# Optimization experiments

Hardware: AMD Instinct MI355X
Metric: run time of the kernel (lower is better)

The kernel has to match this reference:

```python
import jax, jax.numpy as jnp
import numpy as np

TOPK = 5
MAX_CANDIDATES = 32
MAX_LAG_CAP = 168
LN_EPS = 1e-5


def setup_inputs() -> dict:
    key = jax.random.key(0)
    ks = jax.random.split(key, 8)
    B, L, D = 32, 2048, 512
    x = jax.random.normal(ks[0], (B, L, D), dtype=jnp.float32)
    conv_w0 = jax.random.normal(ks[1], (D, 1, 3), dtype=jnp.float32) * 0.1
    conv_w1 = jax.random.normal(ks[2], (D, 1, 5), dtype=jnp.float32) * 0.1
    conv_w2 = jax.random.normal(ks[3], (D, 1, 7), dtype=jnp.float32) * 0.1
    proj_w = jax.random.normal(ks[4], (D, 2 * D), dtype=jnp.float32) * (1.0 / np.sqrt(2 * D))
    proj_b = jnp.zeros((D,), dtype=jnp.float32)
    ln_g = jnp.ones((D,), dtype=jnp.float32)
    ln_b = jnp.zeros((D,), dtype=jnp.float32)
    return {"x": x, "conv_w0": conv_w0, "conv_w1": conv_w1, "conv_w2": conv_w2,
            "proj_w": proj_w, "proj_b": proj_b, "ln_g": ln_g, "ln_b": ln_b}


def _depthwise_conv(x_ncl, w, dilation):
    # x_ncl: [B, D, L], w: [D, 1, k] (torch depthwise layout == OIH with groups=D)
    k = w.shape[-1]
    pad = (k // 2) * dilation
    return jax.lax.conv_general_dilated(
        x_ncl, w, window_strides=(1,), padding=[(pad, pad)],
        rhs_dilation=(dilation,), dimension_numbers=("NCH", "OIH", "NCH"),
        feature_group_count=x_ncl.shape[1])


def _autocorr(x):
    # x: [B, L, D] -> weighted sum of circular shifts at top-k lags
    B, L, D = x.shape
    xm = x.mean(axis=-1)  # [B, L]
    max_lag = min(L - 1, MAX_LAG_CAP)
    num = min(max_lag, MAX_CANDIDATES)
    lags = np.linspace(1, max_lag, num).astype(np.int64)  # static candidate lags
    # score per lag: mean_t xm[:, t] * xm[:, t+lag]
    scores = jnp.stack(
        [(xm[:, : L - int(l)] * xm[:, int(l):]).mean(axis=1) for l in lags], axis=1)  # [B, num]
    k = min(TOPK, num)
    vals, idx = jax.lax.top_k(scores, k)  # [B, k]
    denom = vals.sum(axis=1, keepdims=True) + 1e-6
    # scatter normalized top-k weights onto candidate-lag axis
    w = jnp.zeros((B, num), x.dtype).at[jnp.arange(B)[:, None], idx].add(vals / denom)  # [B, num]
    out = jnp.zeros_like(x)
    for li, lag in enumerate(lags):
        out = out + w[:, li, None, None] * jnp.roll(x, int(lag), axis=1)
    return out


def reference(x, conv_w0, conv_w1, conv_w2, proj_w, proj_b, ln_g, ln_b):
    # depthwise multi-dilation conv branch
    x_T = jnp.transpose(x, (0, 2, 1))  # [B, D, L]
    y_conv = (_depthwise_conv(x_T, conv_w0, 1)
              + _depthwise_conv(x_T, conv_w1, 2)
              + _depthwise_conv(x_T, conv_w2, 4))
    y_conv = jnp.transpose(y_conv, (0, 2, 1))  # [B, L, D]
    # autocorrelation branch
    y_auto = _autocorr(x)
    # project (dropout is identity in eval) + residual + layernorm
    y = jnp.concatenate([y_conv, y_auto], axis=-1)  # [B, L, 2D]
    y = jnp.einsum("bld,od->blo", y, proj_w) + proj_b
    h = x + y
    mu = h.mean(axis=-1, keepdims=True)
    var = h.var(axis=-1, keepdims=True)
    return (h - mu) * jax.lax.rsqrt(var + LN_EPS) * ln_g + ln_b
```

## Files before the change

### kernel.cpp

```cpp
#include <hip/hip_runtime.h>

#define DEVI __device__ __forceinline__

typedef __attribute__((ext_vector_type(8))) short s16x8;
typedef __attribute__((ext_vector_type(4))) float f32x4;

__device__ __constant__ int LAGS_C[32] = {
    1,6,11,17,22,27,33,38,44,49,54,60,65,71,76,81,
    87,92,97,103,108,114,119,124,130,135,141,146,151,157,162,168};

DEVI unsigned short f2bf(float f) {
  unsigned u = __float_as_uint(f);
  return (unsigned short)((u + 0x7FFFu + ((u >> 16) & 1u)) >> 16);
}
DEVI unsigned pk2(float a, float b) {
  return (unsigned)f2bf(a) | ((unsigned)f2bf(b) << 16);
}

DEVI f32x4 mfma16(s16x8 a, s16x8 b, f32x4 c) {
  asm("v_mfma_f32_16x16x32_bf16 %0, %1, %2, %0" : "+v"(c) : "v"(a), "v"(b));
  return c;
}

DEVI void gl_lds16(const void* g, void* l) {
  __builtin_amdgcn_global_load_lds(
      (const __attribute__((address_space(1))) unsigned int*)g,
      (__attribute__((address_space(3))) unsigned int*)l, 16, 0, 0);
}

__global__ __launch_bounds__(256) void k_mean(const float* __restrict__ x,
                                              float* __restrict__ xm) {
  int row = blockIdx.x * 4 + (threadIdx.x >> 6);
  int lane = threadIdx.x & 63;
  const float4* p = (const float4*)(x + (size_t)row * 512 + lane * 8);
  float4 a = p[0], bq = p[1];
  float s = a.x + a.y + a.z + a.w + bq.x + bq.y + bq.z + bq.w;
#pragma unroll
  for (int off = 32; off; off >>= 1) s += __shfl_xor(s, off, 64);
  if (lane == 0) xm[row] = s * (1.0f / 512.0f);
}

__global__ __launch_bounds__(256) void k_cvt(const float* __restrict__ pw,
                                             unsigned short* __restrict__ pwb) {
  int i = (blockIdx.x * 256 + threadIdx.x) * 4;
  float4 v = *(const float4*)(pw + i);
  ushort4 o;
  o.x = f2bf(v.x); o.y = f2bf(v.y); o.z = f2bf(v.z); o.w = f2bf(v.w);
  *(ushort4*)(pwb + i) = o;
}

__global__ __launch_bounds__(256) void k_scores(const float* __restrict__ xm,
                                                float* __restrict__ scores) {
  __shared__ float xs[2048];
  int b = blockIdx.x, tid = threadIdx.x;
  const float4* src = (const float4*)(xm + b * 2048);
  float4* dst = (float4*)xs;
  for (int i = tid; i < 512; i += 256) dst[i] = src[i];
  __syncthreads();
  int wid = tid >> 6, lane = tid & 63;
  for (int j = 0; j < 8; ++j) {
    int li = wid * 8 + j;
    int lag = LAGS_C[li];
    int n = 2048 - lag;
    float p = 0.f;
    for (int t = lane; t < n; t += 64) p += xs[t] * xs[t + lag];
#pragma unroll
    for (int off = 32; off; off >>= 1) p += __shfl_xor(p, off, 64);
    if (lane == 0) scores[b * 32 + li] = p / (float)n;
  }
}

__global__ __launch_bounds__(64) void k_topk(const float* __restrict__ scores,
                                             int* __restrict__ lsel,
                                             float* __restrict__ wsel) {
  int b = threadIdx.x;
  if (b >= 32) return;
  unsigned used = 0;
  int idxs[5];
  float vals[5];
  for (int j = 0; j < 5; ++j) {
    float best = -3.402823466e38f;
    int bi = 0;
    for (int i = 0; i < 32; ++i) {
      float v = scores[b * 32 + i];
      if (!((used >> i) & 1u) && v > best) { best = v; bi = i; }
    }
    used |= 1u << bi;
    idxs[j] = bi;
    vals[j] = best;
  }
  float denom = vals[0] + vals[1] + vals[2] + vals[3] + vals[4] + 1e-6f;
  for (int j = 0; j < 5; ++j) {
    lsel[b * 5 + j] = LAGS_C[idxs[j]];
    wsel[b * 5 + j] = vals[j] / denom;
  }
}

__global__ __launch_bounds__(256) void k_prep(
    const float* __restrict__ x, const float* __restrict__ cw0,
    const float* __restrict__ cw1, const float* __restrict__ cw2,
    const int* __restrict__ lsel, const float* __restrict__ wsel,
    unsigned short* __restrict__ Ab, int b0) {
  __shared__ float xs[88][128];
  __shared__ float cws[15][128];
  const int tid = threadIdx.x;
  const int brel = blockIdx.x >> 7;
  const int t = blockIdx.x & 127;
  const int rt = t >> 2, chg = t & 3;
  const int b = b0 + brel;
  const int l0 = rt << 6;
  const int d0 = chg << 7;
  const float* xb = x + (size_t)b * (2048 * 512);

  for (int idx = tid; idx < 88 * 32; idx += 256) {
    int row = idx >> 5, c4 = idx & 31;
    int l = l0 - 12 + row;
    float4 v = make_float4(0.f, 0.f, 0.f, 0.f);
    if (l >= 0 && l < 2048) v = *(const float4*)(xb + (size_t)l * 512 + d0 + c4 * 4);
    *(float4*)(&xs[row][c4 * 4]) = v;
  }
  for (int idx = tid; idx < 15 * 128; idx += 256) {
    int tap = idx >> 7, ch = idx & 127;
    int d = d0 + ch;
    float v;
    if (tap < 3) v = cw0[d * 3 + tap];
    else if (tap < 8) v = cw1[d * 5 + (tap - 3)];
    else v = cw2[d * 7 + (tap - 8)];
    cws[tap][ch] = v;
  }
  int lag[5];
  float wv[5];
#pragma unroll
  for (int j = 0; j < 5; ++j) {
    lag[j] = lsel[b * 5 + j];
    wv[j] = wsel[b * 5 + j];
  }
  __syncthreads();

  const int ch4 = tid & 31, rbase = tid >> 5;
  constexpr int COFF[15] = {-1, 0, 1, -4, -2, 0, 2, 4, -12, -8, -4, 0, 4, 8, 12};
#pragma unroll 1
  for (int p = 0; p < 8; ++p) {
    int r = p * 8 + rbase;
    float a0 = 0, a1 = 0, a2 = 0, a3 = 0;
#pragma unroll
    for (int tap = 0; tap < 15; ++tap) {
      float4 xv = *(const float4*)(&xs[r + 12 + COFF[tap]][ch4 * 4]);
      float4 wv4 = *(const float4*)(&cws[tap][ch4 * 4]);
      a0 = fmaf(wv4.x, xv.x, a0);
      a1 = fmaf(wv4.y, xv.y, a1);
      a2 = fmaf(wv4.z, xv.z, a2);
      a3 = fmaf(wv4.w, xv.w, a3);
    }
    unsigned short* Arow = Ab + (size_t)(brel * 2048 + l0 + r) * 1024;
    uint2 oc;
    oc.x = pk2(a0, a1);
    oc.y = pk2(a2, a3);
    *(uint2*)(Arow + d0 + ch4 * 4) = oc;
    float s0 = 0, s1 = 0, s2 = 0, s3 = 0;
    int l = l0 + r;
#pragma unroll
    for (int j = 0; j < 5; ++j) {
      int sl = (l - lag[j]) & 2047;
      float4 v = *(const float4*)(xb + (size_t)sl * 512 + d0 + ch4 * 4);
      float w = wv[j];
      s0 = fmaf(w, v.x, s0);
      s1 = fmaf(w, v.y, s1);
      s2 = fmaf(w, v.z, s2);
      s3 = fmaf(w, v.w, s3);
    }
    uint2 oa;
    oa.x = pk2(s0, s1);
    oa.y = pk2(s2, s3);
    *(uint2*)(Arow + 512 + d0 + ch4 * 4) = oa;
  }
}

__global__ __launch_bounds__(512, 1) void k_gemm(
    const unsigned short* __restrict__ Ab, const unsigned short* __restrict__ pwb,
    const float* __restrict__ x, const float* __restrict__ pb,
    const float* __restrict__ lng, const float* __restrict__ lnb,
    float* __restrict__ out, size_t mbase) {
  __shared__ __align__(16) char smem[81920];
  char* Asm = smem;
  char* Bsm = smem + 16384;
  float2* red = (float2*)smem;
  float2* rstat = (float2*)(smem + 4096);

  const int tid = threadIdx.x;
  const int lane = tid & 63;
  const int wid = tid >> 6;
  const int wr = wid >> 2, wc = wid & 3;
  const int lr = lane & 15, g4 = lane >> 4;
  const int m0 = blockIdx.x << 7;

  const int sr = tid >> 2;
  const int ssl = (tid & 3) ^ ((sr >> 1) & 3);
  const unsigned short* aSrc = Ab + (size_t)(m0 + sr) * 1024 + ssl * 8;
  const unsigned short* bSrc0 = pwb + (size_t)sr * 1024 + ssl * 8;

  f32x4 acc[4][8];
#pragma unroll
  for (int m = 0; m < 4; ++m)
#pragma unroll
    for (int n = 0; n < 8; ++n) acc[m][n] = f32x4{0.f, 0.f, 0.f, 0.f};

  const int swsl = (g4 ^ ((lr >> 1) & 3)) << 4;
  const int aoff = (wr * 64 + lr) * 64 + swsl;
  const int boff = (wc * 128 + lr) * 64 + swsl;

#define STAGE(bufi, kt)                                                   \
  do {                                                                    \
    gl_lds16(aSrc + (kt) * 32, Asm + (bufi) * 8192 + wid * 1024);         \
    _Pragma("unroll") for (int i = 0; i < 4; ++i)                         \
        gl_lds16(bSrc0 + (size_t)i * 131072 + (kt) * 32,                  \
                 Bsm + (bufi) * 32768 + i * 8192 + wid * 1024);           \
  } while (0)

  STAGE(0, 0);
  __syncthreads();
#pragma unroll 1
  for (int kt = 0; kt < 32; ++kt) {
    const int cur = kt & 1;
    if (kt + 1 < 32) STAGE(cur ^ 1, kt + 1);
    const char* ab = Asm + cur * 8192;
    const char* bb = Bsm + cur * 32768;
    s16x8 af[4];
#pragma unroll
    for (int m = 0; m < 4; ++m) af[m] = *(const s16x8*)(ab + aoff + m * 1024);
#pragma unroll
    for (int n = 0; n < 8; ++n) {
      s16x8 bf = *(const s16x8*)(bb + boff + n * 1024);
#pragma unroll
      for (int m = 0; m < 4; ++m) acc[m][n] = mfma16(af[m], bf, acc[m][n]);
    }
    __syncthreads();
  }
#undef STAGE

  float pbv[8], gv[8], bv[8];
#pragma unroll
  for (int n = 0; n < 8; ++n) {
    int c = wc * 128 + n * 16 + lr;
    pbv[n] = pb[c];
    gv[n] = lng[c];
    bv[n] = lnb[c];
  }
#pragma unroll
  for (int m = 0; m < 4; ++m) {
#pragma unroll
    for (int reg = 0; reg < 4; ++reg) {
      int row = wr * 64 + m * 16 + g4 * 4 + reg;
      const float* xp = x + (mbase + m0 + row) * 512 + wc * 128 + lr;
      float s1 = 0.f, s2 = 0.f;
#pragma unroll
      for (int n = 0; n < 8; ++n) {
        float h = acc[m][n][reg] + pbv[n] + xp[n * 16];
        acc[m][n][reg] = h;
        s1 += h;
        s2 += h * h;
      }
#pragma unroll
      for (int off = 1; off < 16; off <<= 1) {
        s1 += __shfl_xor(s1, off, 64);
        s2 += __shfl_xor(s2, off, 64);
      }
      if (lr == 0) red[row * 4 + wc] = make_float2(s1, s2);
    }
  }
  __syncthreads();
  if (tid < 128) {
    float s1 = 0.f, s2 = 0.f;
#pragma unroll
    for (int w4 = 0; w4 < 4; ++w4) {
      float2 p = red[tid * 4 + w4];
      s1 += p.x;
      s2 += p.y;
    }
    float mu = s1 * (1.f / 512.f);
    float var = s2 * (1.f / 512.f) - mu * mu;
    rstat[tid] = make_float2(mu, rsqrtf(var + 1e-5f));
  }
  __syncthreads();
#pragma unroll
  for (int m = 0; m < 4; ++m) {
#pragma unroll
    for (int reg = 0; reg < 4; ++reg) {
      int row = wr * 64 + m * 16 + g4 * 4 + reg;
      float2 st = rstat[row];
      float* op = out + (mbase + m0 + row) * 512 + wc * 128 + lr;
#pragma unroll
      for (int n = 0; n < 8; ++n)
        op[n * 16] = (acc[m][n][reg] - st.x) * st.y * gv[n] + bv[n];
    }
  }
}

extern "C" void kernel_launch(void* const* d_in, const int* in_sizes, int n_in,
                              void* d_out, int out_size, void* d_ws, size_t ws_size,
                              hipStream_t stream) {
  const float* x = (const float*)d_in[0];
  const float* cw0 = (const float*)d_in[1];
  const float* cw1 = (const float*)d_in[2];
  const float* cw2 = (const float*)d_in[3];
  const float* pw = (const float*)d_in[4];
  const float* pb = (const float*)d_in[5];
  const float* lng = (const float*)d_in[6];
  const float* lnb = (const float*)d_in[7];
  float* out = (float*)d_out;

  char* ws = (char*)d_ws;
  float* xm = (float*)ws;
  float* scores = (float*)(ws + 262144);
  int* lsel = (int*)(ws + 266240);
  float* wsel = (float*)(ws + 266880);
  unsigned short* pwb = (unsigned short*)(ws + 267520);
  unsigned short* Ab = (unsigned short*)(ws + 1316096);

  size_t avail = ws_size > 1316096 ? ws_size - 1316096 : 0;
  int nch = 1;
  while (nch < 32 && ((size_t)134217728 / nch) > avail) nch <<= 1;
  int bs = 32 / nch;

  k_mean<<<16384, 256, 0, stream>>>(x, xm);
  k_cvt<<<512, 256, 0, stream>>>(pw, pwb);
  k_scores<<<32, 256, 0, stream>>>(xm, scores);
  k_topk<<<1, 64, 0, stream>>>(scores, lsel, wsel);
  for (int c = 0; c < nch; ++c) {
    int b0 = c * bs;
    k_prep<<<bs * 128, 256, 0, stream>>>(x, cw0, cw1, cw2, lsel, wsel, Ab, b0);
    k_gemm<<<bs * 16, 512, 0, stream>>>(Ab, pwb, x, pb, lng, lnb, out,
                                        (size_t)b0 * 2048);
  }
}
```

Measured before the change: 472.9 us.

## Split prep into conv/autocorr kernels, drop batch chunking, retile GEMM to 32 rows

Replaces the combined prep kernel with a separate depthwise-conv kernel that also writes a bf16 copy of x, plus an autocorrelation kernel that gathers the lagged rows from that bf16 copy. The GEMM changes from 128-row tiles with LDS-staged B to 32-row tiles with 256 threads, where each wave loads B fragments straight from global memory. Batch chunking is removed so each stage launches once over all rows. Top-k now keeps its scores in registers. The aim is more parallelism and occupancy, fewer launches and less LDS pressure, at the cost of much more redundant global/L2 traffic for B and a reliance on a large workspace.

```diff
diff --git a/kernel.cpp b/kernel.cpp
--- a/kernel.cpp
+++ b/kernel.cpp
@@ -15,6 +15,9 @@
 }
 DEVI unsigned pk2(float a, float b) {
   return (unsigned)f2bf(a) | ((unsigned)f2bf(b) << 16);
+}
+DEVI float bf2f(unsigned short u) {
+  return __uint_as_float(((unsigned)u) << 16);
 }
 
 DEVI f32x4 mfma16(s16x8 a, s16x8 b, f32x4 c) {
@@ -75,59 +78,124 @@
                                              float* __restrict__ wsel) {
   int b = threadIdx.x;
   if (b >= 32) return;
+  float v[32];
+#pragma unroll
+  for (int i = 0; i < 32; ++i) v[i] = scores[b * 32 + i];
   unsigned used = 0;
   int idxs[5];
   float vals[5];
+#pragma unroll
   for (int j = 0; j < 5; ++j) {
     float best = -3.402823466e38f;
     int bi = 0;
+#pragma unroll
     for (int i = 0; i < 32; ++i) {
-      float v = scores[b * 32 + i];
-      if (!((used >> i) & 1u) && v > best) { best = v; bi = i; }
+      if (!((used >> i) & 1u) && v[i] > best) { best = v[i]; bi = i; }
     }
     used |= 1u << bi;
     idxs[j] = bi;
     vals[j] = best;
   }
   float denom = vals[0] + vals[1] + vals[2] + vals[3] + vals[4] + 1e-6f;
+#pragma unroll
   for (int j = 0; j < 5; ++j) {
     lsel[b * 5 + j] = LAGS_C[idxs[j]];
     wsel[b * 5 + j] = vals[j] / denom;
   }
 }
 
-__global__ __launch_bounds__(256) void k_prep(
+__global__ __launch_bounds__(256) void k_conv(
     const float* __restrict__ x, const float* __restrict__ cw0,
     const float* __restrict__ cw1, const float* __restrict__ cw2,
+    unsigned short* __restrict__ Ab, unsigned short* __restrict__ xbf,
+    int useBf) {
+  __shared__ float xs[40][256];
+  const int tid = threadIdx.x;
+  const int rt = blockIdx.x >> 1, cht = blockIdx.x & 1;
+  const int L0 = rt << 4;
+  const int b = L0 >> 11, l0 = L0 & 2047;
+  const int d0 = cht << 8;
+  const float* xb = x + (size_t)b * (2048 * 512);
+
+#pragma unroll
+  for (int p = 0; p < 10; ++p) {
+    int idx = tid + p * 256;
+    int row = idx >> 6, c = idx & 63;
+    int lb = l0 - 12 + row;
+    float4 v = make_float4(0.f, 0.f, 0.f, 0.f);
+    if (lb >= 0 && lb < 2048) v = *(const float4*)(xb + (size_t)lb * 512 + d0 + c * 4);
+    *(float4*)(&xs[row][c * 4]) = v;
+  }
+
+  const int chg = tid & 63;
+  const int dc = d0 + chg * 4;
+  float r0[12], r1[20], r2[28];
+#pragma unroll
+  for (int i = 0; i < 3; ++i) *(float4*)(&r0[i * 4]) = *(const float4*)(cw0 + dc * 3 + i * 4);
+#pragma unroll
+  for (int i = 0; i < 5; ++i) *(float4*)(&r1[i * 4]) = *(const float4*)(cw1 + dc * 5 + i * 4);
+#pragma unroll
+  for (int i = 0; i < 7; ++i) *(float4*)(&r2[i * 4]) = *(const float4*)(cw2 + dc * 7 + i * 4);
+  float w[15][4];
+#pragma unroll
+  for (int c = 0; c < 4; ++c) {
+#pragma unroll
+    for (int t = 0; t < 3; ++t) w[t][c] = r0[c * 3 + t];
+#pragma unroll
+    for (int t = 0; t < 5; ++t) w[3 + t][c] = r1[c * 5 + t];
+#pragma unroll
+    for (int t = 0; t < 7; ++t) w[8 + t][c] = r2[c * 7 + t];
+  }
+  __syncthreads();
+
+  const int rowg = tid >> 6;
+  const int rbase = rowg << 2;
+  constexpr int COFF[15] = {-1, 0, 1, -4, -2, 0, 2, 4, -12, -8, -4, 0, 4, 8, 12};
+  float acc[4][4];
+#pragma unroll
+  for (int r = 0; r < 4; ++r)
+#pragma unroll
+    for (int c = 0; c < 4; ++c) acc[r][c] = 0.f;
+  float4 xc[4];
+#pragma unroll
+  for (int rr = 0; rr < 28; ++rr) {
+    float4 xv = *(const float4*)(&xs[rbase + rr][chg * 4]);
+    if (rr >= 12 && rr < 16) xc[rr - 12] = xv;
+#pragma unroll
+    for (int tap = 0; tap < 15; ++tap) {
+      const int tr = rr - 12 - COFF[tap];
+      if (tr >= 0 && tr < 4) {
+        acc[tr][0] = fmaf(w[tap][0], xv.x, acc[tr][0]);
+        acc[tr][1] = fmaf(w[tap][1], xv.y, acc[tr][1]);
+        acc[tr][2] = fmaf(w[tap][2], xv.z, acc[tr][2]);
+        acc[tr][3] = fmaf(w[tap][3], xv.w, acc[tr][3]);
+      }
+    }
+  }
+#pragma unroll
+  for (int r = 0; r < 4; ++r) {
+    size_t grow = (size_t)L0 + rbase + r;
+    uint2 oc;
+    oc.x = pk2(acc[r][0], acc[r][1]);
+    oc.y = pk2(acc[r][2], acc[r][3]);
+    *(uint2*)(Ab + grow * 1024 + dc) = oc;
+    if (useBf) {
+      uint2 ox;
+      ox.x = pk2(xc[r].x, xc[r].y);
+      ox.y = pk2(xc[r].z, xc[r].w);
+      *(uint2*)(xbf + grow * 512 + dc) = ox;
+    }
+  }
+}
+
+__global__ __launch_bounds__(256) void k_auto(
+    const float* __restrict__ x, const unsigned short* __restrict__ xbf,
     const int* __restrict__ lsel, const float* __restrict__ wsel,
-    unsigned short* __restrict__ Ab, int b0) {
-  __shared__ float xs[88][128];
-  __shared__ float cws[15][128];
+    unsigned short* __restrict__ Ab, int useBf) {
   const int tid = threadIdx.x;
-  const int brel = blockIdx.x >> 7;
-  const int t = blockIdx.x & 127;
-  const int rt = t >> 2, chg = t & 3;
-  const int b = b0 + brel;
-  const int l0 = rt << 6;
-  const int d0 = chg << 7;
-  const float* xb = x + (size_t)b * (2048 * 512);
-
-  for (int idx = tid; idx < 88 * 32; idx += 256) {
-    int row = idx >> 5, c4 = idx & 31;
-    int l = l0 - 12 + row;
-    float4 v = make_float4(0.f, 0.f, 0.f, 0.f);
-    if (l >= 0 && l < 2048) v = *(const float4*)(xb + (size_t)l * 512 + d0 + c4 * 4);
-    *(float4*)(&xs[row][c4 * 4]) = v;
-  }
-  for (int idx = tid; idx < 15 * 128; idx += 256) {
-    int tap = idx >> 7, ch = idx & 127;
-    int d = d0 + ch;
-    float v;
-    if (tap < 3) v = cw0[d * 3 + tap];
-    else if (tap < 8) v = cw1[d * 5 + (tap - 3)];
-    else v = cw2[d * 7 + (tap - 8)];
-    cws[tap][ch] = v;
-  }
+  const int chg = tid & 63, rowg = tid >> 6;
+  const int L0 = blockIdx.x << 4;
+  const int b = L0 >> 11, lb0 = L0 & 2047;
   int lag[5];
   float wv[5];
 #pragma unroll
@@ -135,86 +203,69 @@
     lag[j] = lsel[b * 5 + j];
     wv[j] = wsel[b * 5 + j];
   }
-  __syncthreads();
-
-  const int ch4 = tid & 31, rbase = tid >> 5;
-  constexpr int COFF[15] = {-1, 0, 1, -4, -2, 0, 2, 4, -12, -8, -4, 0, 4, 8, 12};
-#pragma unroll 1
-  for (int p = 0; p < 8; ++p) {
-    int r = p * 8 + rbase;
-    float a0 = 0, a1 = 0, a2 = 0, a3 = 0;
-#pragma unroll
-    for (int tap = 0; tap < 15; ++tap) {
-      float4 xv = *(const float4*)(&xs[r + 12 + COFF[tap]][ch4 * 4]);
-      float4 wv4 = *(const float4*)(&cws[tap][ch4 * 4]);
-      a0 = fmaf(wv4.x, xv.x, a0);
-      a1 = fmaf(wv4.y, xv.y, a1);
-      a2 = fmaf(wv4.z, xv.z, a2);
-      a3 = fmaf(wv4.w, xv.w, a3);
-    }
-    unsigned short* Arow = Ab + (size_t)(brel * 2048 + l0 + r) * 1024;
-    uint2 oc;
-    oc.x = pk2(a0, a1);
-    oc.y = pk2(a2, a3);
-    *(uint2*)(Arow + d0 + ch4 * 4) = oc;
-    float s0 = 0, s1 = 0, s2 = 0, s3 = 0;
-    int l = l0 + r;
+#pragma unroll
+  for (int r = 0; r < 4; ++r) {
+    int l = lb0 + rowg * 4 + r;
+    float s[8];
+#pragma unroll
+    for (int c = 0; c < 8; ++c) s[c] = 0.f;
 #pragma unroll
     for (int j = 0; j < 5; ++j) {
       int sl = (l - lag[j]) & 2047;
-      float4 v = *(const float4*)(xb + (size_t)sl * 512 + d0 + ch4 * 4);
-      float w = wv[j];
-      s0 = fmaf(w, v.x, s0);
-      s1 = fmaf(w, v.y, s1);
-      s2 = fmaf(w, v.z, s2);
-      s3 = fmaf(w, v.w, s3);
-    }
-    uint2 oa;
-    oa.x = pk2(s0, s1);
-    oa.y = pk2(s2, s3);
-    *(uint2*)(Arow + 512 + d0 + ch4 * 4) = oa;
-  }
-}
-
-__global__ __launch_bounds__(512, 1) void k_gemm(
+      float wj = wv[j];
+      if (useBf) {
+        s16x8 v = *(const s16x8*)(xbf + ((size_t)b * 2048 + sl) * 512 + chg * 8);
+#pragma unroll
+        for (int c = 0; c < 8; ++c)
+          s[c] = fmaf(wj, bf2f((unsigned short)v[c]), s[c]);
+      } else {
+        const float* p = x + ((size_t)b * 2048 + sl) * 512 + chg * 8;
+        float4 lo = *(const float4*)p;
+        float4 hi = *(const float4*)(p + 4);
+        s[0] = fmaf(wj, lo.x, s[0]); s[1] = fmaf(wj, lo.y, s[1]);
+        s[2] = fmaf(wj, lo.z, s[2]); s[3] = fmaf(wj, lo.w, s[3]);
+        s[4] = fmaf(wj, hi.x, s[4]); s[5] = fmaf(wj, hi.y, s[5]);
+        s[6] = fmaf(wj, hi.z, s[6]); s[7] = fmaf(wj, hi.w, s[7]);
+      }
+    }
+    uint4 o;
+    o.x = pk2(s[0], s[1]); o.y = pk2(s[2], s[3]);
+    o.z = pk2(s[4], s[5]); o.w = pk2(s[6], s[7]);
+    *(uint4*)(Ab + (size_t)(L0 + rowg * 4 + r) * 1024 + 512 + chg * 8) = o;
+  }
+}
+
+__global__ __launch_bounds__(256) void k_gemm(
     const unsigned short* __restrict__ Ab, const unsigned short* __restrict__ pwb,
     const float* __restrict__ x, const float* __restrict__ pb,
     const float* __restrict__ lng, const float* __restrict__ lnb,
-    float* __restrict__ out, size_t mbase) {
-  __shared__ __align__(16) char smem[81920];
-  char* Asm = smem;
-  char* Bsm = smem + 16384;
+    float* __restrict__ out) {
+  __shared__ __align__(16) char smem[4096];
   float2* red = (float2*)smem;
-  float2* rstat = (float2*)(smem + 4096);
+  float2* rstat = (float2*)(smem + 1024);
 
   const int tid = threadIdx.x;
   const int lane = tid & 63;
   const int wid = tid >> 6;
-  const int wr = wid >> 2, wc = wid & 3;
   const int lr = lane & 15, g4 = lane >> 4;
-  const int m0 = blockIdx.x << 7;
-
-  const int sr = tid >> 2;
+  const int m0 = blockIdx.x << 5;
+
+  const int sr = (tid & 127) >> 2;
   const int ssl = (tid & 3) ^ ((sr >> 1) & 3);
   const unsigned short* aSrc = Ab + (size_t)(m0 + sr) * 1024 + ssl * 8;
-  const unsigned short* bSrc0 = pwb + (size_t)sr * 1024 + ssl * 8;
-
-  f32x4 acc[4][8];
-#pragma unroll
-  for (int m = 0; m < 4; ++m)
+
+  const int aoff = lr * 64 + ((g4 ^ ((lr >> 1) & 3)) << 4);
+  const unsigned short* bBase = pwb + (size_t)(wid * 128 + lr) * 1024 + g4 * 8;
+
+  f32x4 acc[2][8];
+#pragma unroll
+  for (int m = 0; m < 2; ++m)
 #pragma unroll
     for (int n = 0; n < 8; ++n) acc[m][n] = f32x4{0.f, 0.f, 0.f, 0.f};
 
-  const int swsl = (g4 ^ ((lr >> 1) & 3)) << 4;
-  const int aoff = (wr * 64 + lr) * 64 + swsl;
-  const int boff = (wc * 128 + lr) * 64 + swsl;
-
-#define STAGE(bufi, kt)                                                   \
-  do {                                                                    \
-    gl_lds16(aSrc + (kt) * 32, Asm + (bufi) * 8192 + wid * 1024);         \
-    _Pragma("unroll") for (int i = 0; i < 4; ++i)                         \
-        gl_lds16(bSrc0 + (size_t)i * 131072 + (kt) * 32,                  \
-                 Bsm + (bufi) * 32768 + i * 8192 + wid * 1024);           \
+#define STAGE(b_, kt)                                                   \
+  do {                                                                  \
+    if (wid < 2) gl_lds16(aSrc + (kt) * 32, smem + (b_) * 2048 + wid * 1024); \
   } while (0)
 
   STAGE(0, 0);
@@ -222,17 +273,18 @@
 #pragma unroll 1
   for (int kt = 0; kt < 32; ++kt) {
     const int cur = kt & 1;
-    if (kt + 1 < 32) STAGE(cur ^ 1, kt + 1);
-    const char* ab = Asm + cur * 8192;
-    const char* bb = Bsm + cur * 32768;
-    s16x8 af[4];
-#pragma unroll
-    for (int m = 0; m < 4; ++m) af[m] = *(const s16x8*)(ab + aoff + m * 1024);
+    if (kt < 31) STAGE(cur ^ 1, kt + 1);
+    const char* ab = smem + cur * 2048;
+    s16x8 af0 = *(const s16x8*)(ab + aoff);
+    s16x8 af1 = *(const s16x8*)(ab + aoff + 1024);
+    s16x8 bf[8];
+#pragma unroll
+    for (int n = 0; n < 8; ++n)
+      bf[n] = *(const s16x8*)(bBase + (size_t)n * 16384 + kt * 32);
 #pragma unroll
     for (int n = 0; n < 8; ++n) {
-      s16x8 bf = *(const s16x8*)(bb + boff + n * 1024);
-#pragma unroll
-      for (int m = 0; m < 4; ++m) acc[m][n] = mfma16(af[m], bf, acc[m][n]);
+      acc[0][n] = mfma16(af0, bf[n], acc[0][n]);
+      acc[1][n] = mfma16(af1, bf[n], acc[1][n]);
     }
     __syncthreads();
   }
@@ -241,17 +293,17 @@
   float pbv[8], gv[8], bv[8];
 #pragma unroll
   for (int n = 0; n < 8; ++n) {
-    int c = wc * 128 + n * 16 + lr;
+    int c = wid * 128 + n * 16 + lr;
     pbv[n] = pb[c];
     gv[n] = lng[c];
     bv[n] = lnb[c];
   }
 #pragma unroll
-  for (int m = 0; m < 4; ++m) {
+  for (int m = 0; m < 2; ++m) {
 #pragma unroll
     for (int reg = 0; reg < 4; ++reg) {
-      int row = wr * 64 + m * 16 + g4 * 4 + reg;
-      const float* xp = x + (mbase + m0 + row) * 512 + wc * 128 + lr;
+      int row = m * 16 + g4 * 4 + reg;
+      const float* xp = x + (size_t)(m0 + row) * 512 + wid * 128 + lr;
       float s1 = 0.f, s2 = 0.f;
 #pragma unroll
       for (int n = 0; n < 8; ++n) {
@@ -265,11 +317,11 @@
         s1 += __shfl_xor(s1, off, 64);
         s2 += __shfl_xor(s2, off, 64);
       }
-      if (lr == 0) red[row * 4 + wc] = make_float2(s1, s2);
-    }
-  }
-  __syncthreads();
-  if (tid < 128) {
+      if (lr == 0) red[row * 4 + wid] = make_float2(s1, s2);
+    }
+  }
+  __syncthreads();
+  if (tid < 32) {
     float s1 = 0.f, s2 = 0.f;
 #pragma unroll
     for (int w4 = 0; w4 < 4; ++w4) {
@@ -283,12 +335,12 @@
   }
   __syncthreads();
 #pragma unroll
-  for (int m = 0; m < 4; ++m) {
+  for (int m = 0; m < 2; ++m) {
 #pragma unroll
     for (int reg = 0; reg < 4; ++reg) {
-      int row = wr * 64 + m * 16 + g4 * 4 + reg;
+      int row = m * 16 + g4 * 4 + reg;
       float2 st = rstat[row];
-      float* op = out + (mbase + m0 + row) * 512 + wc * 128 + lr;
+      float* op = out + (size_t)(m0 + row) * 512 + wid * 128 + lr;
 #pragma unroll
       for (int n = 0; n < 8; ++n)
         op[n * 16] = (acc[m][n][reg] - st.x) * st.y * gv[n] + bv[n];
@@ -316,20 +368,15 @@
   float* wsel = (float*)(ws + 266880);
   unsigned short* pwb = (unsigned short*)(ws + 267520);
   unsigned short* Ab = (unsigned short*)(ws + 1316096);
-
-  size_t avail = ws_size > 1316096 ? ws_size - 1316096 : 0;
-  int nch = 1;
-  while (nch < 32 && ((size_t)134217728 / nch) > avail) nch <<= 1;
-  int bs = 32 / nch;
+  unsigned short* xbf = (unsigned short*)(ws + 135533824);
+
+  int useBf = (ws_size >= 202642688ull) ? 1 : 0;
 
   k_mean<<<16384, 256, 0, stream>>>(x, xm);
   k_cvt<<<512, 256, 0, stream>>>(pw, pwb);
+  k_conv<<<8192, 256, 0, stream>>>(x, cw0, cw1, cw2, Ab, xbf, useBf);
   k_scores<<<32, 256, 0, stream>>>(xm, scores);
   k_topk<<<1, 64, 0, stream>>>(scores, lsel, wsel);
-  for (int c = 0; c < nch; ++c) {
-    int b0 = c * bs;
-    k_prep<<<bs * 128, 256, 0, stream>>>(x, cw0, cw1, cw2, lsel, wsel, Ab, b0);
-    k_gemm<<<bs * 16, 512, 0, stream>>>(Ab, pwb, x, pb, lng, lnb, out,
-                                        (size_t)b0 * 2048);
-  }
-}
+  k_auto<<<4096, 256, 0, stream>>>(x, xbf, lsel, wsel, Ab, useBf);
+  k_gemm<<<2048, 256, 0, stream>>>(Ab, pwb, x, pb, lng, lnb, out);
+}
```

After: 660.0 us. 1.4x slower.
